# Optimization experiments

Hardware: AMD Instinct MI355X
Metric: run time of the kernel (lower is better)

## Reference

```python
import jax, jax.numpy as jnp
import numpy as np

TEMPERATURE = 0.5
EPS = 1e-12  # matches torch F.normalize clamp_min


def setup_inputs() -> dict:
    key = jax.random.key(0)
    k1, k2 = jax.random.split(key)
    N, D, C = 8192, 128, 64
    out_1 = jax.random.normal(k1, (N, D), dtype=jnp.float32)
    label = jax.random.randint(k2, (N,), 0, C, dtype=jnp.int64)
    return {"out_1": out_1, "label": label}


def reference(out_1, label):
    N = out_1.shape[0]
    # L2 normalize rows (F.normalize with eps clamp)
    norm = jnp.maximum(jnp.linalg.norm(out_1, axis=-1, keepdims=True), EPS)
    x = out_1 / norm
    # exp-scaled cosine similarity matrix [N, N]
    sim = jnp.exp(jnp.matmul(x, x.T) / TEMPERATURE)
    not_diag = 1.0 - jnp.eye(N, dtype=sim.dtype)
    # negatives: all off-diagonal entries per row
    negative_sim = jnp.sum(sim * not_diag, axis=-1)
    # positives: same label, excluding self; mean per row
    pos_mask = (label[:, None] == label[None, :]).astype(sim.dtype) * not_diag
    pos_count = jnp.sum(pos_mask, axis=-1)
    pos_sim = jnp.sum(sim * pos_mask, axis=-1) / pos_count
    return jnp.mean(-jnp.log(pos_sim / negative_sim))
```

## Files before the change

### kernel.cpp

```cpp
#include <hip/hip_runtime.h>
#include <hip/hip_bf16.h>
#include <stdint.h>

typedef __attribute__((ext_vector_type(8))) __bf16 bf16x8;
typedef __attribute__((ext_vector_type(16))) float floatx16;

#if __has_builtin(__builtin_amdgcn_exp2f)
#define EXP2F(x) __builtin_amdgcn_exp2f(x)
#else
#define EXP2F(x) exp2f(x)
#endif

#define GAS __attribute__((address_space(1)))
#define LAS __attribute__((address_space(3)))

#define SCALE_SQRT 1.69864359f
#define JCH 16
#define JPB 8

__global__ __launch_bounds__(256) void k_sort1(const int* __restrict__ raw,
                                               int* __restrict__ lab,
                                               int* __restrict__ ranks,
                                               int* __restrict__ cnt, int N) {
  __shared__ int h[64];
  __shared__ int s64;
  const int r = blockIdx.x * 256 + threadIdx.x;
  if (threadIdx.x < 64) {
    h[threadIdx.x] = 0;
    const int probe = raw[2 * threadIdx.x + 1];
    const unsigned long long b = __ballot(probe != 0);
    if (threadIdx.x == 0) s64 = (b == 0ull);
  }
  __syncthreads();
  const int l = (s64 ? raw[2 * r] : raw[r]) & 63;
  lab[r] = l;
  ranks[r] = atomicAdd(&h[l], 1);
  __syncthreads();
  if (threadIdx.x < 64) cnt[blockIdx.x * 64 + threadIdx.x] = h[threadIdx.x];
}

__global__ __launch_bounds__(256) void k_scan(const int* __restrict__ cnt,
                                              int* __restrict__ base,
                                              int* __restrict__ cum, int N) {
  __shared__ int tot[64];
  const int k = threadIdx.x;
  const int nch = N >> 8;
  if (k < 64) {
    int run = 0;
    for (int c = 0; c < nch; ++c) { base[c * 64 + k] = run; run += cnt[c * 64 + k]; }
    tot[k] = run;
  }
  __syncthreads();
  if (k == 0) {
    int run = 0;
    for (int i = 0; i < 64; ++i) { cum[i] = run; run += tot[i]; }
    cum[64] = run;
  }
  __syncthreads();
  for (int i = threadIdx.x; i < nch * 64; i += 256) base[i] += cum[i & 63];
}

__global__ __launch_bounds__(256) void k_prep(const float* __restrict__ x,
                                              const int* __restrict__ lab,
                                              const int* __restrict__ ranks,
                                              const int* __restrict__ base,
                                              ushort* __restrict__ xb,
                                              int* __restrict__ labs, int N) {
  const int row = (blockIdx.x * 256 + threadIdx.x) >> 6;
  const int lane = threadIdx.x & 63;
  if (row >= N) return;
  const int l = lab[row];
  const int slot = base[(row >> 8) * 64 + l] + ranks[row];
  const float2 v = ((const float2*)(x + (size_t)row * 128))[lane];
  float ss = v.x * v.x + v.y * v.y;
#pragma unroll
  for (int m = 1; m < 64; m <<= 1) ss += __shfl_xor(ss, m, 64);
  const float rn = SCALE_SQRT / fmaxf(sqrtf(ss), 1e-12f);
  __hip_bfloat162 o;
  o.x = __float2bfloat16(v.x * rn);
  o.y = __float2bfloat16(v.y * rn);
  ((__hip_bfloat162*)xb)[slot * 64 + lane] = o;
  if (lane == 0) labs[slot] = l;
}

__global__ __launch_bounds__(256, 3) void k_sim(const ushort* __restrict__ xb,
                                                const int* __restrict__ labs,
                                                const int* __restrict__ cum,
                                                float* __restrict__ pneg,
                                                float* __restrict__ ppos, int N) {
  __shared__ ushort ldsB[2][64 * 128];
  const int tid = threadIdx.x;
  const int lane = tid & 63;
  const int wv = tid >> 6;
  const int l31 = lane & 31, g2 = lane >> 5;
  const int l15 = lane & 15, g4 = lane >> 4;
  const int i0 = blockIdx.y * 128;
  const int c = blockIdx.x;
  const int jt0 = c * JPB;

  {
    const int jrow0 = jt0 * 64;
#pragma unroll
    for (int it = 0; it < 4; ++it) {
      const int r0 = it * 16 + wv * 4;
      const int lr = r0 + g4;
      const int kb = l15 ^ (lr & 15);
      const ushort* gp = xb + (size_t)(jrow0 + lr) * 128 + kb * 8;
      __builtin_amdgcn_global_load_lds((GAS void*)gp, (LAS void*)&ldsB[0][r0 * 128], 16, 0, 0);
    }
  }

  bf16x8 afr[8];
  {
    const ushort* arow_p = xb + (size_t)(i0 + wv * 32 + l31) * 128 + g2 * 8;
#pragma unroll
    for (int kt = 0; kt < 8; ++kt)
      afr[kt] = *(const bf16x8*)(arow_p + kt * 16);
  }

  const int wps = cum[labs[i0 + wv * 32]];
  const int wpe = cum[labs[i0 + wv * 32 + 31] + 1];

  int li_pack[4] = {0, 0, 0, 0};
#pragma unroll
  for (int t = 0; t < 16; ++t) {
    const int r = (t & 3) + 8 * (t >> 2) + 4 * g2;
    li_pack[t >> 2] |= labs[i0 + wv * 32 + r] << ((t & 3) * 8);
  }

  int baddr[8];
#pragma unroll
  for (int kt = 0; kt < 8; ++kt)
    baddr[kt] = l31 * 128 + (((kt * 2 + g2) ^ l15) * 8);

  float neg[16], pos[16];
#pragma unroll
  for (int t = 0; t < 16; ++t) { neg[t] = 0.0f; pos[t] = 0.0f; }

  __syncthreads();

  for (int t = 0; t < JPB; ++t) {
    const int j0 = (jt0 + t) * 64;
    const ushort* bbase = (t & 1) ? ldsB[1] : ldsB[0];
    ushort* bnext = (t & 1) ? ldsB[0] : ldsB[1];
    if (t + 1 < JPB) {
#pragma unroll
      for (int it = 0; it < 4; ++it) {
        const int r0 = it * 16 + wv * 4;
        const int lr = r0 + g4;
        const int kb = l15 ^ (lr & 15);
        const ushort* gp = xb + (size_t)(j0 + 64 + lr) * 128 + kb * 8;
        __builtin_amdgcn_global_load_lds((GAS void*)gp, (LAS void*)&bnext[r0 * 128], 16, 0, 0);
      }
    }

    floatx16 acc0 = (floatx16)(0.0f), acc1 = (floatx16)(0.0f);
#pragma unroll
    for (int kt = 0; kt < 8; ++kt) {
      const bf16x8 b0 = *(const bf16x8*)&bbase[baddr[kt]];
      const bf16x8 b1 = *(const bf16x8*)&bbase[baddr[kt] + 32 * 128];
      acc0 = __builtin_amdgcn_mfma_f32_32x32x16_bf16(afr[kt], b0, acc0, 0, 0, 0);
      acc1 = __builtin_amdgcn_mfma_f32_32x32x16_bf16(afr[kt], b1, acc1, 0, 0, 0);
    }

    const bool posT = (j0 < wpe) && (j0 + 64 > wps);
    if (!posT) {
#pragma unroll
      for (int reg = 0; reg < 16; ++reg)
        neg[reg] += EXP2F(acc0[reg]) + EXP2F(acc1[reg]);
    } else {
      const int lj0 = labs[j0 + l31];
      const int lj1 = labs[j0 + 32 + l31];
      const int dlt = j0 - (i0 + wv * 32);
      const bool dg = (dlt > -64) && (dlt < 32);
#pragma unroll
      for (int reg = 0; reg < 16; ++reg) {
        float e0 = EXP2F(acc0[reg]);
        float e1 = EXP2F(acc1[reg]);
        if (dg) {
          const int ir = (reg & 3) + 8 * (reg >> 2) + 4 * g2;
          if (ir == dlt + l31) e0 = 0.0f;
          if (ir == dlt + 32 + l31) e1 = 0.0f;
        }
        const int liq = (li_pack[reg >> 2] >> ((reg & 3) * 8)) & 63;
        neg[reg] += e0 + e1;
        pos[reg] += (liq == lj0 ? e0 : 0.0f) + (liq == lj1 ? e1 : 0.0f);
      }
    }
    __syncthreads();
  }

#pragma unroll
  for (int t = 0; t < 16; ++t) {
    float n = neg[t], p = pos[t];
#pragma unroll
    for (int m = 1; m < 32; m <<= 1) {
      n += __shfl_xor(n, m, 64);
      p += __shfl_xor(p, m, 64);
    }
    if (l31 == 0) {
      const int r = i0 + wv * 32 + (t & 3) + 8 * (t >> 2) + 4 * g2;
      pneg[(size_t)c * N + r] = n;
      ppos[(size_t)c * N + r] = p;
    }
  }
}

__global__ __launch_bounds__(1024) void k_final(const float* __restrict__ pneg,
                                                const float* __restrict__ ppos,
                                                const int* __restrict__ labs,
                                                const int* __restrict__ cum,
                                                float* __restrict__ out, int N) {
  double s = 0.0;
  for (int i = threadIdx.x; i < N; i += 1024) {
    float n = 0.0f, p = 0.0f;
#pragma unroll
    for (int c = 0; c < JCH; ++c) {
      n += pneg[(size_t)c * N + i];
      p += ppos[(size_t)c * N + i];
    }
    const int l = labs[i];
    const float cnt = (float)(cum[l + 1] - cum[l] - 1);
    s += (double)logf(n * cnt / p);
  }
#pragma unroll
  for (int m = 1; m < 64; m <<= 1) s += __shfl_xor(s, m, 64);
  __shared__ double wsum[16];
  if ((threadIdx.x & 63) == 0) wsum[threadIdx.x >> 6] = s;
  __syncthreads();
  if (threadIdx.x == 0) {
    double tot = 0.0;
    for (int w = 0; w < 16; ++w) tot += wsum[w];
    out[0] = (float)(tot / (double)N);
  }
}

extern "C" void kernel_launch(void* const* d_in, const int* in_sizes, int n_in,
                              void* d_out, int out_size, void* d_ws, size_t ws_size,
                              hipStream_t stream) {
  const float* x = (const float*)d_in[0];
  const int* raw_label = (const int*)d_in[1];
  const int N = in_sizes[1];
  char* ws = (char*)d_ws;
  ushort* xb = (ushort*)ws;
  float* pneg = (float*)(ws + (size_t)N * 128 * 2);
  float* ppos = pneg + (size_t)JCH * N;
  int* lab = (int*)(ppos + (size_t)JCH * N);
  int* ranks = lab + N;
  int* labs = ranks + N;
  int* cnt = labs + N;
  int* base = cnt + (N >> 8) * 64;
  int* cum = base + (N >> 8) * 64;
  float* out = (float*)d_out;

  k_sort1<<<dim3(N / 256), dim3(256), 0, stream>>>(raw_label, lab, ranks, cnt, N);
  k_scan<<<dim3(1), dim3(256), 0, stream>>>(cnt, base, cum, N);
  k_prep<<<dim3(N / 4), dim3(256), 0, stream>>>(x, lab, ranks, base, xb, labs, N);
  k_sim<<<dim3(JCH, N / 128), dim3(256), 0, stream>>>(xb, labs, cum, pneg, ppos, N);
  k_final<<<dim3(1), dim3(1024), 0, stream>>>(pneg, ppos, labs, cum, out, N);
}
```

Baseline: 114.7 us.

## Load B fragments directly from pre-swizzled global layout, drop LDS staging

The prep kernel now also writes a second bf16 copy of the normalized rows, arranged so that each wave can load MFMA B fragments with one contiguous 16-byte load per lane. The similarity kernel drops the shared-memory double buffer and its block barriers. Each wave streams its own 32-column tiles from global memory or L2 into registers with a one-tile register prefetch, using a single 32x32 accumulator per step. In exchange it doubles the workspace writes in prep, and each of the four waves now fetches the same B tiles separately instead of sharing them through LDS.

```diff
diff --git a/kernel.cpp b/kernel.cpp
--- a/kernel.cpp
+++ b/kernel.cpp
@@ -11,12 +11,9 @@
 #define EXP2F(x) exp2f(x)
 #endif
 
-#define GAS __attribute__((address_space(1)))
-#define LAS __attribute__((address_space(3)))
-
 #define SCALE_SQRT 1.69864359f
 #define JCH 16
-#define JPB 8
+#define TPW 16
 
 __global__ __launch_bounds__(256) void k_sort1(const int* __restrict__ raw,
                                                int* __restrict__ lab,
@@ -65,6 +62,7 @@
                                               const int* __restrict__ ranks,
                                               const int* __restrict__ base,
                                               ushort* __restrict__ xb,
+                                              ushort* __restrict__ xb2,
                                               int* __restrict__ labs, int N) {
   const int row = (blockIdx.x * 256 + threadIdx.x) >> 6;
   const int lane = threadIdx.x & 63;
@@ -80,114 +78,92 @@
   o.x = __float2bfloat16(v.x * rn);
   o.y = __float2bfloat16(v.y * rn);
   ((__hip_bfloat162*)xb)[slot * 64 + lane] = o;
+  const int kt = lane >> 3;
+  const int g2b = (lane >> 2) & 1;
+  const int e = (2 * lane) & 7;
+  const int jt = slot >> 5, n = slot & 31;
+  ((__hip_bfloat162*)xb2)[(jt * 8 + kt) * 256 + (g2b * 32 + n) * 4 + (e >> 1)] = o;
   if (lane == 0) labs[slot] = l;
 }
 
 __global__ __launch_bounds__(256, 3) void k_sim(const ushort* __restrict__ xb,
+                                                const ushort* __restrict__ xb2,
                                                 const int* __restrict__ labs,
                                                 const int* __restrict__ cum,
                                                 float* __restrict__ pneg,
                                                 float* __restrict__ ppos, int N) {
-  __shared__ ushort ldsB[2][64 * 128];
   const int tid = threadIdx.x;
   const int lane = tid & 63;
   const int wv = tid >> 6;
   const int l31 = lane & 31, g2 = lane >> 5;
-  const int l15 = lane & 15, g4 = lane >> 4;
   const int i0 = blockIdx.y * 128;
+  const int rowbase = i0 + wv * 32;
   const int c = blockIdx.x;
-  const int jt0 = c * JPB;
-
-  {
-    const int jrow0 = jt0 * 64;
-#pragma unroll
-    for (int it = 0; it < 4; ++it) {
-      const int r0 = it * 16 + wv * 4;
-      const int lr = r0 + g4;
-      const int kb = l15 ^ (lr & 15);
-      const ushort* gp = xb + (size_t)(jrow0 + lr) * 128 + kb * 8;
-      __builtin_amdgcn_global_load_lds((GAS void*)gp, (LAS void*)&ldsB[0][r0 * 128], 16, 0, 0);
-    }
-  }
+  const int j0base = c * (TPW * 32);
 
   bf16x8 afr[8];
   {
-    const ushort* arow_p = xb + (size_t)(i0 + wv * 32 + l31) * 128 + g2 * 8;
-#pragma unroll
-    for (int kt = 0; kt < 8; ++kt)
-      afr[kt] = *(const bf16x8*)(arow_p + kt * 16);
-  }
-
-  const int wps = cum[labs[i0 + wv * 32]];
-  const int wpe = cum[labs[i0 + wv * 32 + 31] + 1];
+    const ushort* ap = xb + (size_t)(rowbase + l31) * 128 + g2 * 8;
+#pragma unroll
+    for (int kt = 0; kt < 8; ++kt) afr[kt] = *(const bf16x8*)(ap + kt * 16);
+  }
+
+  const int wps = cum[labs[rowbase]];
+  const int wpe = cum[labs[rowbase + 31] + 1];
 
   int li_pack[4] = {0, 0, 0, 0};
 #pragma unroll
   for (int t = 0; t < 16; ++t) {
     const int r = (t & 3) + 8 * (t >> 2) + 4 * g2;
-    li_pack[t >> 2] |= labs[i0 + wv * 32 + r] << ((t & 3) * 8);
-  }
-
-  int baddr[8];
+    li_pack[t >> 2] |= labs[rowbase + r] << ((t & 3) * 8);
+  }
+
+  float neg[16], pos[16];
+#pragma unroll
+  for (int t = 0; t < 16; ++t) { neg[t] = 0.0f; pos[t] = 0.0f; }
+
+  const ushort* bbase = xb2 + (size_t)(j0base >> 5) * 4096 + lane * 8;
+
+  bf16x8 bfr[8];
 #pragma unroll
   for (int kt = 0; kt < 8; ++kt)
-    baddr[kt] = l31 * 128 + (((kt * 2 + g2) ^ l15) * 8);
-
-  float neg[16], pos[16];
-#pragma unroll
-  for (int t = 0; t < 16; ++t) { neg[t] = 0.0f; pos[t] = 0.0f; }
-
-  __syncthreads();
-
-  for (int t = 0; t < JPB; ++t) {
-    const int j0 = (jt0 + t) * 64;
-    const ushort* bbase = (t & 1) ? ldsB[1] : ldsB[0];
-    ushort* bnext = (t & 1) ? ldsB[0] : ldsB[1];
-    if (t + 1 < JPB) {
-#pragma unroll
-      for (int it = 0; it < 4; ++it) {
-        const int r0 = it * 16 + wv * 4;
-        const int lr = r0 + g4;
-        const int kb = l15 ^ (lr & 15);
-        const ushort* gp = xb + (size_t)(j0 + 64 + lr) * 128 + kb * 8;
-        __builtin_amdgcn_global_load_lds((GAS void*)gp, (LAS void*)&bnext[r0 * 128], 16, 0, 0);
-      }
-    }
-
-    floatx16 acc0 = (floatx16)(0.0f), acc1 = (floatx16)(0.0f);
-#pragma unroll
-    for (int kt = 0; kt < 8; ++kt) {
-      const bf16x8 b0 = *(const bf16x8*)&bbase[baddr[kt]];
-      const bf16x8 b1 = *(const bf16x8*)&bbase[baddr[kt] + 32 * 128];
-      acc0 = __builtin_amdgcn_mfma_f32_32x32x16_bf16(afr[kt], b0, acc0, 0, 0, 0);
-      acc1 = __builtin_amdgcn_mfma_f32_32x32x16_bf16(afr[kt], b1, acc1, 0, 0, 0);
-    }
-
-    const bool posT = (j0 < wpe) && (j0 + 64 > wps);
+    bfr[kt] = *(const bf16x8*)(bbase + kt * 512);
+
+  for (int t = 0; t < TPW; ++t) {
+    const int j0 = j0base + t * 32;
+
+    floatx16 acc = (floatx16)(0.0f);
+#pragma unroll
+    for (int kt = 0; kt < 8; ++kt)
+      acc = __builtin_amdgcn_mfma_f32_32x32x16_bf16(afr[kt], bfr[kt], acc, 0, 0, 0);
+
+    if (t + 1 < TPW) {
+      const ushort* bn = bbase + (size_t)(t + 1) * 4096;
+#pragma unroll
+      for (int kt = 0; kt < 8; ++kt)
+        bfr[kt] = *(const bf16x8*)(bn + kt * 512);
+    }
+
+    const bool posT = (j0 < wpe) && (j0 + 32 > wps);
     if (!posT) {
 #pragma unroll
       for (int reg = 0; reg < 16; ++reg)
-        neg[reg] += EXP2F(acc0[reg]) + EXP2F(acc1[reg]);
+        neg[reg] += EXP2F(acc[reg]);
     } else {
-      const int lj0 = labs[j0 + l31];
-      const int lj1 = labs[j0 + 32 + l31];
-      const int dlt = j0 - (i0 + wv * 32);
-      const bool dg = (dlt > -64) && (dlt < 32);
+      const int lj = labs[j0 + l31];
+      const bool dg = (j0 == rowbase);
 #pragma unroll
       for (int reg = 0; reg < 16; ++reg) {
-        float e0 = EXP2F(acc0[reg]);
-        float e1 = EXP2F(acc1[reg]);
+        float e = EXP2F(acc[reg]);
         if (dg) {
           const int ir = (reg & 3) + 8 * (reg >> 2) + 4 * g2;
-          if (ir == dlt + l31) e0 = 0.0f;
-          if (ir == dlt + 32 + l31) e1 = 0.0f;
+          if (ir == l31) e = 0.0f;
         }
         const int liq = (li_pack[reg >> 2] >> ((reg & 3) * 8)) & 63;
-        neg[reg] += e0 + e1;
-        pos[reg] += (liq == lj0 ? e0 : 0.0f) + (liq == lj1 ? e1 : 0.0f);
+        neg[reg] += e;
+        pos[reg] += (liq == lj) ? e : 0.0f;
       }
     }
-    __syncthreads();
   }
 
 #pragma unroll
@@ -199,7 +175,7 @@
       p += __shfl_xor(p, m, 64);
     }
     if (l31 == 0) {
-      const int r = i0 + wv * 32 + (t & 3) + 8 * (t >> 2) + 4 * g2;
+      const int r = rowbase + (t & 3) + 8 * (t >> 2) + 4 * g2;
       pneg[(size_t)c * N + r] = n;
       ppos[(size_t)c * N + r] = p;
     }
@@ -243,7 +219,8 @@
   const int N = in_sizes[1];
   char* ws = (char*)d_ws;
   ushort* xb = (ushort*)ws;
-  float* pneg = (float*)(ws + (size_t)N * 128 * 2);
+  ushort* xb2 = xb + (size_t)N * 128;
+  float* pneg = (float*)(xb2 + (size_t)N * 128);
   float* ppos = pneg + (size_t)JCH * N;
   int* lab = (int*)(ppos + (size_t)JCH * N);
   int* ranks = lab + N;
@@ -255,7 +232,7 @@
 
   k_sort1<<<dim3(N / 256), dim3(256), 0, stream>>>(raw_label, lab, ranks, cnt, N);
   k_scan<<<dim3(1), dim3(256), 0, stream>>>(cnt, base, cum, N);
-  k_prep<<<dim3(N / 4), dim3(256), 0, stream>>>(x, lab, ranks, base, xb, labs, N);
-  k_sim<<<dim3(JCH, N / 128), dim3(256), 0, stream>>>(xb, labs, cum, pneg, ppos, N);
+  k_prep<<<dim3(N / 4), dim3(256), 0, stream>>>(x, lab, ranks, base, xb, xb2, labs, N);
+  k_sim<<<dim3(JCH, N / 128), dim3(256), 0, stream>>>(xb, xb2, labs, cum, pneg, ppos, N);
   k_final<<<dim3(1), dim3(1024), 0, stream>>>(pneg, ppos, labs, cum, out, N);
 }
```

Result: slower. 117.3 us (+2.3%).
